# Performance work log

Measured on AMD Instinct MI355X. Metric: run time of the kernel, lower is better.

Reference implementation:

```python
import jax, jax.numpy as jnp
import numpy as np

LN_EPS = 1e-5
NUM_HEADS = 16

def _layernorm(x, g, b):
    mu = jnp.mean(x, axis=-1, keepdims=True)
    var = jnp.mean(jnp.square(x - mu), axis=-1, keepdims=True)
    return (x - mu) * jax.lax.rsqrt(var + LN_EPS) * g + b

def setup_inputs() -> dict:
    key = jax.random.key(0)
    ks = jax.random.split(key, 8)
    B, N, C, Hf = 8, 4096, 1024, 2048
    s = 1.0 / np.sqrt(C)
    return {
        "x": jax.random.normal(ks[0], (B, N, C), jnp.float32),
        "ln1_g": jnp.ones((C,), jnp.float32),
        "ln1_b": jnp.zeros((C,), jnp.float32),
        "ln2_g": jnp.ones((C,), jnp.float32),
        "ln2_b": jnp.zeros((C,), jnp.float32),
        "wq": jax.random.normal(ks[1], (C, C), jnp.float32) * s,
        "wk": jax.random.normal(ks[2], (C, C), jnp.float32) * s,
        "wv": jax.random.normal(ks[3], (C, C), jnp.float32) * s,
        "proj_w": jax.random.normal(ks[4], (C, C), jnp.float32) * s,
        "proj_b": jnp.zeros((C,), jnp.float32),
        "fc1_w": jax.random.normal(ks[5], (C, Hf), jnp.float32) * s,
        "fc1_b": jnp.zeros((Hf,), jnp.float32),
        "fc2_w": jax.random.normal(ks[6], (Hf, C), jnp.float32) / np.sqrt(Hf),
        "fc2_b": jnp.zeros((C,), jnp.float32),
    }

def reference(x, ln1_g, ln1_b, ln2_g, ln2_b, wq, wk, wv, proj_w, proj_b,
              fc1_w, fc1_b, fc2_w, fc2_b):
    B, N, C = x.shape
    H = NUM_HEADS
    d = C // H
    scale = d ** -0.5

    # --- attention branch (note: attention over the head_dim axis, d x d scores) ---
    h = _layernorm(x, ln1_g, ln1_b)
    def split(t):  # (B,N,C) -> (B,H,d,N), matching permute(0,2,3,1)
        return jnp.transpose(t.reshape(B, N, H, d), (0, 2, 3, 1))
    q = split(h @ wq)
    k = split(h @ wk)
    v = split(h @ wv)
    attn = jax.nn.softmax(jnp.einsum("bhdn,bhen->bhde", q, k) * scale, axis=-1)  # (B,H,d,d)
    o = jnp.einsum("bhde,bhen->bhdn", attn, v)           # (B,H,d,N)
    o = jnp.transpose(o, (0, 2, 1, 3)).reshape(B, N, C)  # transpose(1,2).reshape
    x = x + (o @ proj_w + proj_b)

    # --- MLP branch ---
    h2 = _layernorm(x, ln2_g, ln2_b)
    h2 = jax.nn.gelu(h2 @ fc1_w + fc1_b, approximate=False)
    x = x + (h2 @ fc2_w + fc2_b)
    return x
```

## Files before the change

### kernel.cpp

```cpp
#include <hip/hip_runtime.h>
#include <cmath>

typedef __attribute__((ext_vector_type(8))) _Float16 f16x8;
typedef __attribute__((ext_vector_type(8))) unsigned short u16x8;
typedef __attribute__((ext_vector_type(4))) float f32x4;

__device__ __forceinline__ unsigned short f2h(float f) {
  return __builtin_bit_cast(unsigned short, (_Float16)f);
}
__device__ __forceinline__ float h2f(unsigned short u) {
  return (float)__builtin_bit_cast(_Float16, u);
}

__device__ __forceinline__ void async16(const void* gp, void* lp) {
  __builtin_amdgcn_global_load_lds(
      (const __attribute__((address_space(1))) void*)gp,
      (__attribute__((address_space(3))) void*)lp, 16, 0, 0);
}

struct TCArgs {
  const float* W[6];
  unsigned short* T[6];
  int K[6];
  int N[6];
};

__global__ __launch_bounds__(256) void transpose_cast6(TCArgs a) {
  const int z = blockIdx.z;
  const int K = a.K[z], N = a.N[z];
  const int n0 = blockIdx.x * 32, k0 = blockIdx.y * 32;
  if (n0 >= N || k0 >= K) return;
  const float* __restrict__ W = a.W[z];
  unsigned short* __restrict__ WT = a.T[z];
  __shared__ float tile[32][33];
  const int tx = threadIdx.x & 31, ty = threadIdx.x >> 5;
#pragma unroll
  for (int r = 0; r < 4; ++r)
    tile[ty + 8 * r][tx] = W[(size_t)(k0 + ty + 8 * r) * N + n0 + tx];
  __syncthreads();
#pragma unroll
  for (int r = 0; r < 4; ++r)
    WT[(size_t)(n0 + ty + 8 * r) * K + k0 + tx] = f2h(tile[tx][ty + 8 * r]);
}

__global__ __launch_bounds__(256) void layernorm_cast(
    const float* __restrict__ x, const float* __restrict__ g,
    const float* __restrict__ bt, unsigned short* __restrict__ out) {
  const int row = blockIdx.x, tid = threadIdx.x;
  const float4 v = ((const float4*)(x + (size_t)row * 1024))[tid];
  float s = v.x + v.y + v.z + v.w;
  float ss = v.x * v.x + v.y * v.y + v.z * v.z + v.w * v.w;
#pragma unroll
  for (int off = 32; off >= 1; off >>= 1) {
    s += __shfl_down(s, off);
    ss += __shfl_down(ss, off);
  }
  __shared__ float red[10];
  const int wave = tid >> 6, lane = tid & 63;
  if (lane == 0) { red[wave] = s; red[4 + wave] = ss; }
  __syncthreads();
  if (tid == 0) {
    float S = red[0] + red[1] + red[2] + red[3];
    float SS = red[4] + red[5] + red[6] + red[7];
    float mu = S * (1.f / 1024.f);
    float var = SS * (1.f / 1024.f) - mu * mu;
    red[8] = mu;
    red[9] = rsqrtf(var + 1e-5f);
  }
  __syncthreads();
  const float mu = red[8], rs = red[9];
  const float4 gv = ((const float4*)g)[tid];
  const float4 bv = ((const float4*)bt)[tid];
  ushort4 r;
  r.x = f2h((v.x - mu) * rs * gv.x + bv.x);
  r.y = f2h((v.y - mu) * rs * gv.y + bv.y);
  r.z = f2h((v.z - mu) * rs * gv.z + bv.z);
  r.w = f2h((v.w - mu) * rs * gv.w + bv.w);
  ((ushort4*)(out + (size_t)row * 1024))[tid] = r;
}

__global__ __launch_bounds__(256) void resid_ln(
    const float* __restrict__ x, const unsigned short* __restrict__ pr,
    const float* __restrict__ pb, const float* __restrict__ g,
    const float* __restrict__ bt, float* __restrict__ out,
    unsigned short* __restrict__ h2) {
  const int row = blockIdx.x, tid = threadIdx.x;
  const size_t off = (size_t)row * 1024;
  const float4 xv = ((const float4*)(x + off))[tid];
  const ushort4 pv = ((const ushort4*)(pr + off))[tid];
  const float4 bb = ((const float4*)pb)[tid];
  float4 v;
  v.x = xv.x + h2f(pv.x) + bb.x;
  v.y = xv.y + h2f(pv.y) + bb.y;
  v.z = xv.z + h2f(pv.z) + bb.z;
  v.w = xv.w + h2f(pv.w) + bb.w;
  ((float4*)(out + off))[tid] = v;
  float s = v.x + v.y + v.z + v.w;
  float ss = v.x * v.x + v.y * v.y + v.z * v.z + v.w * v.w;
#pragma unroll
  for (int o = 32; o >= 1; o >>= 1) {
    s += __shfl_down(s, o);
    ss += __shfl_down(ss, o);
  }
  __shared__ float red[10];
  const int wave = tid >> 6, lane = tid & 63;
  if (lane == 0) { red[wave] = s; red[4 + wave] = ss; }
  __syncthreads();
  if (tid == 0) {
    float S = red[0] + red[1] + red[2] + red[3];
    float SS = red[4] + red[5] + red[6] + red[7];
    float mu = S * (1.f / 1024.f);
    float var = SS * (1.f / 1024.f) - mu * mu;
    red[8] = mu;
    red[9] = rsqrtf(var + 1e-5f);
  }
  __syncthreads();
  const float mu = red[8], rs = red[9];
  const float4 gv = ((const float4*)g)[tid];
  const float4 bv = ((const float4*)bt)[tid];
  ushort4 r;
  r.x = f2h((v.x - mu) * rs * gv.x + bv.x);
  r.y = f2h((v.y - mu) * rs * gv.y + bv.y);
  r.z = f2h((v.z - mu) * rs * gv.z + bv.z);
  r.w = f2h((v.w - mu) * rs * gv.w + bv.w);
  ((ushort4*)(h2 + off))[tid] = r;
}

__global__ __launch_bounds__(256) void resid_add(
    float* __restrict__ out, const unsigned short* __restrict__ y,
    const float* __restrict__ b) {
  const int row = blockIdx.x, tid = threadIdx.x;
  const size_t off = (size_t)row * 1024;
  float4 o = ((const float4*)(out + off))[tid];
  const ushort4 yv = ((const ushort4*)(y + off))[tid];
  const float4 bv = ((const float4*)b)[tid];
  o.x += h2f(yv.x) + bv.x;
  o.y += h2f(yv.y) + bv.y;
  o.z += h2f(yv.z) + bv.z;
  o.w += h2f(yv.w) + bv.w;
  ((float4*)(out + off))[tid] = o;
}


#define STAGE_A(TT, KKH)                                                       \
  {                                                                            \
    unsigned short* d = smem + ((TT) & 1) * 32768 + (KKH) * 8192 + wave * 512; \
    const unsigned short* sp_ = pA + (size_t)(TT) * 64 + (KKH) * 32;           \
    async16(sp_, d);                                                           \
    async16(sp_ + rstep, d + 4096);                                            \
  }

#define STAGE_B(TT, KKH)                                                       \
  {                                                                            \
    unsigned short* d =                                                        \
        smem + ((TT) & 1) * 32768 + 16384 + (KKH) * 8192 + wave * 512;         \
    const unsigned short* sp_ = pB + (size_t)(TT) * 64 + (KKH) * 32;           \
    async16(sp_, d);                                                           \
    async16(sp_ + rstep, d + 4096);                                            \
  }

#define GPHASE(KK, MH, STAGE, TAILW)                                           \
  {                                                                            \
    f16x8 af[4];                                                               \
    _Pragma("unroll") for (int i = 0; i < 4; ++i) {                            \
      const int ra = wm * 128 + ((MH)*4 + i) * 16 + l16;                       \
      af[i] = __builtin_bit_cast(                                              \
          f16x8, *(const u16x8*)&bufA[(KK)*8192 + ra * 32 +                    \
                                      ((g16 ^ ((ra >> 1) & 3)) * 8)]);         \
    }                                                                          \
    if ((MH) == 0) {                                                           \
      _Pragma("unroll") for (int j = 0; j < 4; ++j) {                          \
        const int rb = wn * 64 + j * 16 + l16;                                 \
        bf[j] = __builtin_bit_cast(                                            \
            f16x8, *(const u16x8*)&bufB[(KK)*8192 + rb * 32 +                  \
                                        ((g16 ^ ((rb >> 1) & 3)) * 8)]);       \
      }                                                                        \
    }                                                                          \
    STAGE;                                                                     \
    __builtin_amdgcn_s_barrier();                                              \
    asm volatile("s_waitcnt lgkmcnt(0)" ::: "memory");                         \
    __builtin_amdgcn_s_setprio(1);                                             \
    _Pragma("unroll") for (int i = 0; i < 4; ++i)                              \
        _Pragma("unroll") for (int j = 0; j < 4; ++j) acc[(MH)*4 + i][j] =     \
        __builtin_amdgcn_mfma_f32_16x16x32_f16(af[i], bf[j],                   \
                                               acc[(MH)*4 + i][j], 0, 0, 0);   \
    __builtin_amdgcn_s_setprio(0);                                             \
    TAILW;                                                                     \
    __builtin_amdgcn_s_barrier();                                              \
  }

__global__ __launch_bounds__(512) void gemm256(
    const unsigned short* __restrict__ A, const unsigned short* __restrict__ BT,
    int M, int N, int K,
    const float* __restrict__ bias, unsigned short* __restrict__ outB, int gelu) {
  __shared__ __align__(16) unsigned short smem[65536];
  const int tid = threadIdx.x, wave = tid >> 6, lane = tid & 63;
  const int l16 = lane & 15, g16 = lane >> 4;
  const int wm = wave >> 2, wn = wave & 3;

  const int lin = blockIdx.y * gridDim.x + blockIdx.x;
  const int t_ = lin >> 3;
  const int bx = t_ % gridDim.x;
  const int by = (lin & 7) + 8 * (t_ / gridDim.x);
  const int row0 = by * 256, col0 = bx * 256;

  const int r_ = tid >> 2;
  const int s_ = ((tid & 3) ^ ((tid >> 3) & 3)) * 8;
  const unsigned short* pA = A + (size_t)(row0 + r_) * K + s_;
  const unsigned short* pB = BT + (size_t)(col0 + r_) * K + s_;
  const size_t rstep = (size_t)128 * K;
  const int NT = K >> 6;

  f32x4 acc[8][4] = {};

  STAGE_B(0, 0);
  STAGE_A(0, 0);
  STAGE_B(0, 1);
  STAGE_A(0, 1);
  STAGE_B(1, 0);
  STAGE_A(1, 0);
  STAGE_B(1, 1);
  asm volatile("s_waitcnt vmcnt(6)" ::: "memory");
  __builtin_amdgcn_s_barrier();

  for (int t = 0; t < NT - 2; ++t) {
    const unsigned short* bufA = smem + (t & 1) * 32768;
    const unsigned short* bufB = bufA + 16384;
    f16x8 bf[4];
    GPHASE(0, 0, STAGE_A(t + 1, 1), )
    GPHASE(0, 1, STAGE_B(t + 2, 0), )
    GPHASE(1, 0, STAGE_A(t + 2, 0), )
    GPHASE(1, 1, STAGE_B(t + 2, 1),
           asm volatile("s_waitcnt vmcnt(6)" ::: "memory"))
  }

  {
    const int t = NT - 2;
    const unsigned short* bufA = smem + (t & 1) * 32768;
    const unsigned short* bufB = bufA + 16384;
    f16x8 bf[4];
    GPHASE(0, 0, STAGE_A(t + 1, 1), )
    GPHASE(0, 1, , )
    GPHASE(1, 0, , )
    GPHASE(1, 1, , asm volatile("s_waitcnt vmcnt(0)" ::: "memory"))
  }
  {
    const int t = NT - 1;
    const unsigned short* bufA = smem + (t & 1) * 32768;
    const unsigned short* bufB = bufA + 16384;
    f16x8 bf[4];
    GPHASE(0, 0, , )
    GPHASE(0, 1, , )
    GPHASE(1, 0, , )
    GPHASE(1, 1, , )
  }

  unsigned short* scr = smem + wave * 4352;
#pragma unroll
  for (int mh = 0; mh < 2; ++mh) {
#pragma unroll
    for (int j = 0; j < 4; ++j) {
      const float bcol = gelu ? bias[col0 + wn * 64 + j * 16 + l16] : 0.f;
#pragma unroll
      for (int i = 0; i < 4; ++i)
#pragma unroll
        for (int r = 0; r < 4; ++r) {
          float val = acc[mh * 4 + i][j][r] + bcol;
          if (gelu) val = 0.5f * val * (1.0f + erff(val * 0.70710678118f));
          scr[(i * 16 + g16 * 4 + r) * 68 + j * 16 + l16] = f2h(val);
        }
    }
#pragma unroll
    for (int rr = 0; rr < 8; ++rr) {
      const int lr = rr * 8 + (lane >> 3);
      const int lc = (lane & 7) * 8;
      const u16x8 val = *(const u16x8*)&scr[lr * 68 + lc];
      *(u16x8*)(outB + (size_t)(row0 + wm * 128 + mh * 64 + lr) * N + col0 +
                wn * 64 + lc) = val;
    }
  }
}

__global__ __launch_bounds__(256) void attn_qk_part(
    const unsigned short* __restrict__ qkv, float* __restrict__ sp) {
  constexpr int ST = 72;
  __shared__ unsigned short sQT[64 * ST];
  __shared__ unsigned short sKT[64 * ST];
  const int bx = blockIdx.x, bh = bx >> 2, chunk = bx & 3;
  const int b = bh >> 4, h = bh & 15;
  const size_t base = (size_t)b * 4096 * 3072 + (size_t)h * 64;
  const int tid = threadIdx.x, wave = tid >> 6, lane = tid & 63;
  const int l16 = lane & 15, g16 = lane >> 4;
  const int wm = wave & 1, wn = wave >> 1;
  const int srow = tid >> 2, sseg = tid & 3;

  f32x4 acc[2][2] = {};

  for (int ntl = 0; ntl < 16; ++ntl) {
    const int nt = chunk * 16 + ntl;
    __syncthreads();
    const size_t roff = base + (size_t)(nt * 64 + srow) * 3072 + sseg * 16;
    const u16x8 q0 = *(const u16x8*)(qkv + roff);
    const u16x8 q1 = *(const u16x8*)(qkv + roff + 8);
    const u16x8 k0 = *(const u16x8*)(qkv + roff + 1024);
    const u16x8 k1 = *(const u16x8*)(qkv + roff + 1032);
#pragma unroll
    for (int ii = 0; ii < 8; ++ii) {
      sQT[(sseg * 16 + ii) * ST + srow] = q0[ii];
      sQT[(sseg * 16 + 8 + ii) * ST + srow] = q1[ii];
      sKT[(sseg * 16 + ii) * ST + srow] = k0[ii];
      sKT[(sseg * 16 + 8 + ii) * ST + srow] = k1[ii];
    }
    __syncthreads();
#pragma unroll
    for (int kk = 0; kk < 2; ++kk) {
      f16x8 aq[2], bk[2];
#pragma unroll
      for (int i = 0; i < 2; ++i)
        aq[i] = __builtin_bit_cast(f16x8,
            *(const u16x8*)&sQT[(wm * 32 + i * 16 + l16) * ST + kk * 32 + g16 * 8]);
#pragma unroll
      for (int j = 0; j < 2; ++j)
        bk[j] = __builtin_bit_cast(f16x8,
            *(const u16x8*)&sKT[(wn * 32 + j * 16 + l16) * ST + kk * 32 + g16 * 8]);
#pragma unroll
      for (int i = 0; i < 2; ++i)
#pragma unroll
        for (int j = 0; j < 2; ++j)
          acc[i][j] = __builtin_amdgcn_mfma_f32_16x16x32_f16(aq[i], bk[j], acc[i][j], 0, 0, 0);
    }
  }

  float* o = sp + (size_t)bx * 4096;
#pragma unroll
  for (int i = 0; i < 2; ++i)
#pragma unroll
    for (int j = 0; j < 2; ++j)
#pragma unroll
      for (int r = 0; r < 4; ++r)
        o[(wm * 32 + i * 16 + g16 * 4 + r) * 64 + (wn * 32 + j * 16 + l16)] = acc[i][j][r];
}

__global__ __launch_bounds__(256) void attn_softmax(
    const float* __restrict__ sp, unsigned short* __restrict__ am) {
  const int gid = blockIdx.x * 4 + (threadIdx.x >> 6);
  const int lane = threadIdx.x & 63;
  const int bh = gid >> 6, dd = gid & 63;
  const float* p = sp + (size_t)bh * 16384 + dd * 64 + lane;
  const float v = p[0] + p[4096] + p[8192] + p[12288];
  float mx = v;
#pragma unroll
  for (int o = 32; o >= 1; o >>= 1) mx = fmaxf(mx, __shfl_xor(mx, o));
  const float e = __expf(0.125f * (v - mx));
  float s = e;
#pragma unroll
  for (int o = 32; o >= 1; o >>= 1) s += __shfl_xor(s, o);
  am[(size_t)bh * 4096 + dd * 64 + lane] = f2h(e / s);
}

__global__ __launch_bounds__(256) void attn_pv(
    const unsigned short* __restrict__ qkv, const unsigned short* __restrict__ am,
    unsigned short* __restrict__ o) {
  const int bx = blockIdx.x, bh = bx >> 2, chunk = bx & 3;
  const int b = bh >> 4, h = bh & 15;
  const size_t base = (size_t)b * 4096 * 3072 + (size_t)h * 64;
  const int tid = threadIdx.x, wave = tid >> 6, lane = tid & 63;
  const int l16 = lane & 15, g16 = lane >> 4;
  const int wm = wave & 1, wn = wave >> 1;

  f16x8 amf[2][2];
#pragma unroll
  for (int i = 0; i < 2; ++i)
#pragma unroll
    for (int kk = 0; kk < 2; ++kk)
      amf[i][kk] = __builtin_bit_cast(f16x8,
          *(const u16x8*)(am + (size_t)bh * 4096 +
                          (wm * 32 + i * 16 + l16) * 64 + kk * 32 + g16 * 8));

  for (int ntl = 0; ntl < 16; ++ntl) {
    const int nt = chunk * 16 + ntl;
    f32x4 oc[2][2] = {};
#pragma unroll
    for (int kk = 0; kk < 2; ++kk) {
#pragma unroll
      for (int j = 0; j < 2; ++j) {
        const f16x8 vf = __builtin_bit_cast(f16x8,
            *(const u16x8*)(qkv + base + 2048 +
                            (size_t)(nt * 64 + wn * 32 + j * 16 + l16) * 3072 +
                            kk * 32 + g16 * 8));
#pragma unroll
        for (int i = 0; i < 2; ++i)
          oc[i][j] = __builtin_amdgcn_mfma_f32_16x16x32_f16(amf[i][kk], vf, oc[i][j], 0, 0, 0);
      }
    }
#pragma unroll
    for (int i = 0; i < 2; ++i)
#pragma unroll
      for (int j = 0; j < 2; ++j)
#pragma unroll
        for (int r = 0; r < 4; ++r) {
          const int dd = wm * 32 + i * 16 + g16 * 4 + r;
          const int nf = nt * 64 + wn * 32 + j * 16 + l16;
          const int row = b * 4096 + dd * 64 + h * 4 + (nf >> 10);
          o[(size_t)row * 1024 + (nf & 1023)] = f2h(oc[i][j][r]);
        }
  }
}

extern "C" void kernel_launch(void* const* d_in, const int* in_sizes, int n_in,
                              void* d_out, int out_size, void* d_ws, size_t ws_size,
                              hipStream_t stream) {
  (void)in_sizes; (void)n_in; (void)out_size; (void)ws_size;
  const float* x = (const float*)d_in[0];
  const float* ln1g = (const float*)d_in[1];
  const float* ln1b = (const float*)d_in[2];
  const float* ln2g = (const float*)d_in[3];
  const float* ln2b = (const float*)d_in[4];
  const float* wq = (const float*)d_in[5];
  const float* wk = (const float*)d_in[6];
  const float* wv = (const float*)d_in[7];
  const float* projw = (const float*)d_in[8];
  const float* projb = (const float*)d_in[9];
  const float* fc1w = (const float*)d_in[10];
  const float* fc1b = (const float*)d_in[11];
  const float* fc2w = (const float*)d_in[12];
  const float* fc2b = (const float*)d_in[13];
  float* out = (float*)d_out;

  const int M = 8 * 4096, C = 1024, HF = 2048;
  const size_t MC = (size_t)M * C;

  unsigned short* p = (unsigned short*)d_ws;
  unsigned short* wqkvT = p; p += (size_t)3 * C * C;
  unsigned short* prT = p; p += (size_t)C * C;
  unsigned short* f1T = p; p += (size_t)HF * C;
  unsigned short* f2T = p; p += (size_t)C * HF;
  unsigned short* hb = p;  p += MC;
  unsigned short* qkvb = p; p += 3 * MC;
  float* Spart = (float*)hb;
  unsigned short* Am = wqkvT;
  unsigned short* ob = hb;
  unsigned short* projout = qkvb;
  unsigned short* h2 = qkvb + 2 * MC;
  unsigned short* h3 = qkvb;
  unsigned short* yb = hb;

  TCArgs ta;
  ta.W[0] = wq;    ta.T[0] = wqkvT;                     ta.K[0] = C;  ta.N[0] = C;
  ta.W[1] = wk;    ta.T[1] = wqkvT + (size_t)C * C;     ta.K[1] = C;  ta.N[1] = C;
  ta.W[2] = wv;    ta.T[2] = wqkvT + (size_t)2 * C * C; ta.K[2] = C;  ta.N[2] = C;
  ta.W[3] = projw; ta.T[3] = prT;                       ta.K[3] = C;  ta.N[3] = C;
  ta.W[4] = fc1w;  ta.T[4] = f1T;                       ta.K[4] = C;  ta.N[4] = HF;
  ta.W[5] = fc2w;  ta.T[5] = f2T;                       ta.K[5] = HF; ta.N[5] = C;
  transpose_cast6<<<dim3(HF / 32, HF / 32, 6), 256, 0, stream>>>(ta);

  layernorm_cast<<<M, 256, 0, stream>>>(x, ln1g, ln1b, hb);

  gemm256<<<dim3(3 * C / 256, M / 256), 512, 0, stream>>>(
      hb, wqkvT, M, 3 * C, C, nullptr, qkvb, 0);

  attn_qk_part<<<512, 256, 0, stream>>>(qkvb, Spart);
  attn_softmax<<<2048, 256, 0, stream>>>(Spart, Am);
  attn_pv<<<512, 256, 0, stream>>>(qkvb, Am, ob);

  gemm256<<<dim3(C / 256, M / 256), 512, 0, stream>>>(
      ob, prT, M, C, C, nullptr, projout, 0);

  resid_ln<<<M, 256, 0, stream>>>(x, projout, projb, ln2g, ln2b, out, h2);

  gemm256<<<dim3(HF / 256, M / 256), 512, 0, stream>>>(
      h2, f1T, M, HF, C, fc1b, h3, 1);

  gemm256<<<dim3(C / 256, M / 256), 512, 0, stream>>>(
      h3, f2T, M, C, HF, nullptr, yb, 0);

  resid_add<<<M, 256, 0, stream>>>(out, yb, fc2b);
}
```

Measured before the change: 1.145 ms.

## Fuse final residual add into fc2 GEMM epilogue and coalesce attn_pv stores

The separate resid_add kernel is removed, and the fc2 GEMM epilogue now adds the fp16 result plus bias directly into the fp32 output. This saves a launch and one read and write of the intermediate buffer. attn_pv now stages its output tile through LDS so it can issue 16-byte row stores instead of scattered 2-byte stores. sched_barrier fences are added around the staging and MFMA phases of the GEMM loop to pin instruction ordering, which could also constrain the compiler's scheduling.

```diff
diff --git a/kernel.cpp b/kernel.cpp
--- a/kernel.cpp
+++ b/kernel.cpp
@@ -126,21 +126,6 @@
   ((ushort4*)(h2 + off))[tid] = r;
 }
 
-__global__ __launch_bounds__(256) void resid_add(
-    float* __restrict__ out, const unsigned short* __restrict__ y,
-    const float* __restrict__ b) {
-  const int row = blockIdx.x, tid = threadIdx.x;
-  const size_t off = (size_t)row * 1024;
-  float4 o = ((const float4*)(out + off))[tid];
-  const ushort4 yv = ((const ushort4*)(y + off))[tid];
-  const float4 bv = ((const float4*)b)[tid];
-  o.x += h2f(yv.x) + bv.x;
-  o.y += h2f(yv.y) + bv.y;
-  o.z += h2f(yv.z) + bv.z;
-  o.w += h2f(yv.w) + bv.w;
-  ((float4*)(out + off))[tid] = o;
-}
-
 
 #define STAGE_A(TT, KKH)                                                       \
   {                                                                            \
@@ -176,15 +161,19 @@
                                         ((g16 ^ ((rb >> 1) & 3)) * 8)]);       \
       }                                                                        \
     }                                                                          \
+    __builtin_amdgcn_sched_barrier(0);                                         \
     STAGE;                                                                     \
+    __builtin_amdgcn_sched_barrier(0);                                         \
     __builtin_amdgcn_s_barrier();                                              \
     asm volatile("s_waitcnt lgkmcnt(0)" ::: "memory");                         \
+    __builtin_amdgcn_sched_barrier(0);                                         \
     __builtin_amdgcn_s_setprio(1);                                             \
     _Pragma("unroll") for (int i = 0; i < 4; ++i)                              \
         _Pragma("unroll") for (int j = 0; j < 4; ++j) acc[(MH)*4 + i][j] =     \
         __builtin_amdgcn_mfma_f32_16x16x32_f16(af[i], bf[j],                   \
                                                acc[(MH)*4 + i][j], 0, 0, 0);   \
     __builtin_amdgcn_s_setprio(0);                                             \
+    __builtin_amdgcn_sched_barrier(0);                                         \
     TAILW;                                                                     \
     __builtin_amdgcn_s_barrier();                                              \
   }
@@ -192,7 +181,8 @@
 __global__ __launch_bounds__(512) void gemm256(
     const unsigned short* __restrict__ A, const unsigned short* __restrict__ BT,
     int M, int N, int K,
-    const float* __restrict__ bias, unsigned short* __restrict__ outB, int gelu) {
+    const float* __restrict__ bias, unsigned short* __restrict__ outB, int gelu,
+    float* __restrict__ resid, const float* __restrict__ rbias) {
   __shared__ __align__(16) unsigned short smem[65536];
   const int tid = threadIdx.x, wave = tid >> 6, lane = tid & 63;
   const int l16 = lane & 15, g16 = lane >> 4;
@@ -220,6 +210,7 @@
   STAGE_B(1, 0);
   STAGE_A(1, 0);
   STAGE_B(1, 1);
+  __builtin_amdgcn_sched_barrier(0);
   asm volatile("s_waitcnt vmcnt(6)" ::: "memory");
   __builtin_amdgcn_s_barrier();
 
@@ -270,13 +261,39 @@
           scr[(i * 16 + g16 * 4 + r) * 68 + j * 16 + l16] = f2h(val);
         }
     }
-#pragma unroll
-    for (int rr = 0; rr < 8; ++rr) {
-      const int lr = rr * 8 + (lane >> 3);
-      const int lc = (lane & 7) * 8;
-      const u16x8 val = *(const u16x8*)&scr[lr * 68 + lc];
-      *(u16x8*)(outB + (size_t)(row0 + wm * 128 + mh * 64 + lr) * N + col0 +
-                wn * 64 + lc) = val;
+    if (resid) {
+#pragma unroll
+      for (int rr = 0; rr < 8; ++rr) {
+        const int lr = rr * 8 + (lane >> 3);
+        const int lc = (lane & 7) * 8;
+        const u16x8 val = *(const u16x8*)&scr[lr * 68 + lc];
+        const int grow = row0 + wm * 128 + mh * 64 + lr;
+        const int gcol = col0 + wn * 64 + lc;
+        float* po = resid + (size_t)grow * N + gcol;
+        const float4 b0 = ((const float4*)(rbias + gcol))[0];
+        const float4 b1 = ((const float4*)(rbias + gcol))[1];
+        float4 o0 = ((const float4*)po)[0];
+        float4 o1 = ((const float4*)po)[1];
+        o0.x += h2f(val[0]) + b0.x;
+        o0.y += h2f(val[1]) + b0.y;
+        o0.z += h2f(val[2]) + b0.z;
+        o0.w += h2f(val[3]) + b0.w;
+        o1.x += h2f(val[4]) + b1.x;
+        o1.y += h2f(val[5]) + b1.y;
+        o1.z += h2f(val[6]) + b1.z;
+        o1.w += h2f(val[7]) + b1.w;
+        ((float4*)po)[0] = o0;
+        ((float4*)po)[1] = o1;
+      }
+    } else {
+#pragma unroll
+      for (int rr = 0; rr < 8; ++rr) {
+        const int lr = rr * 8 + (lane >> 3);
+        const int lc = (lane & 7) * 8;
+        const u16x8 val = *(const u16x8*)&scr[lr * 68 + lc];
+        *(u16x8*)(outB + (size_t)(row0 + wm * 128 + mh * 64 + lr) * N + col0 +
+                  wn * 64 + lc) = val;
+      }
     }
   }
 }
@@ -361,12 +378,14 @@
 __global__ __launch_bounds__(256) void attn_pv(
     const unsigned short* __restrict__ qkv, const unsigned short* __restrict__ am,
     unsigned short* __restrict__ o) {
+  __shared__ unsigned short pvs[4 * 1088];
   const int bx = blockIdx.x, bh = bx >> 2, chunk = bx & 3;
   const int b = bh >> 4, h = bh & 15;
   const size_t base = (size_t)b * 4096 * 3072 + (size_t)h * 64;
   const int tid = threadIdx.x, wave = tid >> 6, lane = tid & 63;
   const int l16 = lane & 15, g16 = lane >> 4;
   const int wm = wave & 1, wn = wave >> 1;
+  unsigned short* tw = pvs + wave * 1088;
 
   f16x8 amf[2][2];
 #pragma unroll
@@ -393,17 +412,24 @@
           oc[i][j] = __builtin_amdgcn_mfma_f32_16x16x32_f16(amf[i][kk], vf, oc[i][j], 0, 0, 0);
       }
     }
+    asm volatile("s_waitcnt lgkmcnt(0)" ::: "memory");
 #pragma unroll
     for (int i = 0; i < 2; ++i)
 #pragma unroll
       for (int j = 0; j < 2; ++j)
 #pragma unroll
-        for (int r = 0; r < 4; ++r) {
-          const int dd = wm * 32 + i * 16 + g16 * 4 + r;
-          const int nf = nt * 64 + wn * 32 + j * 16 + l16;
-          const int row = b * 4096 + dd * 64 + h * 4 + (nf >> 10);
-          o[(size_t)row * 1024 + (nf & 1023)] = f2h(oc[i][j][r]);
-        }
+        for (int r = 0; r < 4; ++r)
+          tw[(i * 16 + g16 * 4 + r) * 34 + j * 16 + l16] = f2h(oc[i][j][r]);
+    asm volatile("s_waitcnt lgkmcnt(0)" ::: "memory");
+    const int rt = lane >> 1;
+    const int c0 = (lane & 1) * 16;
+#pragma unroll
+    for (int c2 = 0; c2 < 2; ++c2) {
+      const int ct = c0 + c2 * 8;
+      const u16x8 v8 = *(const u16x8*)&tw[rt * 34 + ct];
+      const int row = b * 4096 + (wm * 32 + rt) * 64 + h * 4 + chunk;
+      *(u16x8*)(o + (size_t)row * 1024 + ntl * 64 + wn * 32 + ct) = v8;
+    }
   }
 }
 
@@ -457,22 +483,20 @@
   layernorm_cast<<<M, 256, 0, stream>>>(x, ln1g, ln1b, hb);
 
   gemm256<<<dim3(3 * C / 256, M / 256), 512, 0, stream>>>(
-      hb, wqkvT, M, 3 * C, C, nullptr, qkvb, 0);
+      hb, wqkvT, M, 3 * C, C, nullptr, qkvb, 0, nullptr, nullptr);
 
   attn_qk_part<<<512, 256, 0, stream>>>(qkvb, Spart);
   attn_softmax<<<2048, 256, 0, stream>>>(Spart, Am);
   attn_pv<<<512, 256, 0, stream>>>(qkvb, Am, ob);
 
   gemm256<<<dim3(C / 256, M / 256), 512, 0, stream>>>(
-      ob, prT, M, C, C, nullptr, projout, 0);
+      ob, prT, M, C, C, nullptr, projout, 0, nullptr, nullptr);
 
   resid_ln<<<M, 256, 0, stream>>>(x, projout, projb, ln2g, ln2b, out, h2);
 
   gemm256<<<dim3(HF / 256, M / 256), 512, 0, stream>>>(
-      h2, f1T, M, HF, C, fc1b, h3, 1);
+      h2, f1T, M, HF, C, fc1b, h3, 1, nullptr, nullptr);
 
   gemm256<<<dim3(C / 256, M / 256), 512, 0, stream>>>(
-      h3, f2T, M, C, HF, nullptr, yb, 0);
-
-  resid_add<<<M, 256, 0, stream>>>(out, yb, fc2b);
-}
+      h3, f2T, M, C, HF, nullptr, yb, 0, out, fc2b);
+}
```

Result: faster. 1.096 ms (-4.3%).
